# Kernel optimization log

Hardware: AMD Instinct MI355X
Metric: run time of the kernel (lower is better)

Reference implementation:

```python
import jax, jax.numpy as jnp
import numpy as np

H, C = 4, 64          # heads, per-head out_channels (hidden_dim // heads)
D = 256               # hidden_dim
DE = 128              # edge_dim
N_ROWS, N_TOKENS, E = 20000, 100000, 300000
SCALE = 1.0 / np.sqrt(C).astype(np.float32)
EPS = 1e-5


def _lin(key, din, dout):
    k1, k2 = jax.random.split(key)
    W = jax.random.normal(k1, (din, dout), jnp.float32) * 0.05
    b = jax.random.normal(k2, (dout,), jnp.float32) * 0.05
    return W, b


def setup_inputs() -> dict:
    key = jax.random.key(0)
    ks = jax.random.split(key, 26)
    inp = {
        "row_x": jax.random.normal(ks[0], (N_ROWS, D), jnp.float32),
        "token_x": jax.random.normal(ks[1], (N_TOKENS, D), jnp.float32),
        "t2r_edge_index": jax.random.randint(ks[2], (2, E), 0, N_ROWS, jnp.int64),
        "edge_attr_t2r": jax.random.normal(ks[3], (E, DE), jnp.float32),
        "r2t_edge_index": jax.random.randint(ks[4], (2, E), 0, N_ROWS, jnp.int64),
        "edge_attr_r2t": jax.random.normal(ks[5], (E, DE), jnp.float32),
    }
    i = 6
    for p in ("t2r", "r2t"):
        for nm, din in (("q", D), ("k", D), ("v", D), ("e", DE), ("s", D)):
            W, b = _lin(ks[i], din, D); i += 1
            inp[p + "_W" + nm] = W
            inp[p + "_b" + nm] = b
    inp["row_gamma"] = jnp.ones((D,), jnp.float32)
    inp["row_beta"] = jnp.zeros((D,), jnp.float32)
    inp["token_gamma"] = jnp.ones((D,), jnp.float32)
    inp["token_beta"] = jnp.zeros((D,), jnp.float32)
    return inp


def _transformer_conv(x_src, x_dst, ei, ea, Wq, bq, Wk, bk, Wv, bv, We, be, Ws, bs):
    """PyG TransformerConv (concat=True, root_weight=True, edge_dim set, eval)."""
    N = x_dst.shape[0]
    q = (x_dst @ Wq + bq).reshape(N, H, C)       # [N_dst,H,C]
    k = (x_src @ Wk + bk).reshape(-1, H, C)      # [N_src,H,C]
    v = (x_src @ Wv + bv).reshape(-1, H, C)
    e = (ea @ We + be).reshape(-1, H, C)         # [E,H,C]
    src, dst = ei[0], ei[1]
    kj = k[src] + e                              # key_j + edge
    logits = jnp.einsum('ehc,ehc->eh', q[dst], kj) * SCALE  # [E,H]
    amax = jax.ops.segment_max(logits, dst, num_segments=N)  # [N,H]
    ex = jnp.exp(logits - amax[dst])
    denom = jax.ops.segment_sum(ex, dst, num_segments=N)
    alpha = ex / denom[dst]                      # segment softmax over dst
    msg = jax.ops.segment_sum((v[src] + e) * alpha[..., None], dst, num_segments=N)
    return msg.reshape(N, H * C) + x_dst @ Ws + bs  # concat heads + skip lin


def _ln(x, g, b):
    m = jnp.mean(x, -1, keepdims=True)
    var = jnp.mean(jnp.square(x - m), -1, keepdims=True)
    return (x - m) * jax.lax.rsqrt(var + EPS) * g + b


def reference(row_x, token_x, t2r_edge_index, edge_attr_t2r, r2t_edge_index, edge_attr_r2t,
              t2r_Wq, t2r_bq, t2r_Wk, t2r_bk, t2r_Wv, t2r_bv, t2r_We, t2r_be, t2r_Ws, t2r_bs,
              r2t_Wq, r2t_bq, r2t_Wk, r2t_bk, r2t_Wv, r2t_bv, r2t_We, r2t_be, r2t_Ws, r2t_bs,
              row_gamma, row_beta, token_gamma, token_beta):
    row_msg = _transformer_conv(token_x, row_x, t2r_edge_index, edge_attr_t2r,
                                t2r_Wq, t2r_bq, t2r_Wk, t2r_bk, t2r_Wv, t2r_bv,
                                t2r_We, t2r_be, t2r_Ws, t2r_bs)
    row_out = _ln(row_x + row_msg, row_gamma, row_beta)
    tok_msg = _transformer_conv(row_out, token_x, r2t_edge_index, edge_attr_r2t,
                                r2t_Wq, r2t_bq, r2t_Wk, r2t_bk, r2t_Wv, r2t_bv,
                                r2t_We, r2t_be, r2t_Ws, r2t_bs)
    token_out = _ln(token_x + tok_msg, token_gamma, token_beta)
    return row_out, token_out
```

## Files before the change

### kernel.cpp

```cpp
#include <hip/hip_runtime.h>
#include <cstdint>
#include <cstddef>

#define NMAX 100000
#define EMAX 300000

typedef __bf16 bf16_t;
typedef __bf16 bf16x8 __attribute__((ext_vector_type(8)));
typedef float f32x4 __attribute__((ext_vector_type(4)));
typedef unsigned int u32;

__device__ unsigned short g_mega[(size_t)NMAX * 1024];
__device__ unsigned short g_qs [(size_t)NMAX * 512];
__device__ unsigned short g_kv [(size_t)NMAX * 512];
__device__ unsigned short g_eb1[(size_t)EMAX * 256];
__device__ unsigned short g_eb2[(size_t)EMAX * 256];
__device__ unsigned short g_bfA[(size_t)NMAX * 256];
__device__ unsigned short g_bfB[(size_t)NMAX * 256];
__device__ unsigned short g_bfW[589824];
__device__ float g_bias[2560];
__device__ int   g_deg [NMAX + 1];
__device__ int   g_rowptr[NMAX + 1];
__device__ int   g_cur [NMAX];
__device__ int2  g_perm2[EMAX];
__device__ int   g_bsum[512];

struct P4  { const float* p[4]; };
struct P10 { const float* p[10]; };

__device__ __forceinline__ unsigned short f2bf(float f) {
  unsigned u = __float_as_uint(f);
  return (unsigned short)((u + 0x7fffu + ((u >> 16) & 1u)) >> 16);
}
__device__ __forceinline__ void dec8(uint4 u, float* f) {
  f[0] = __uint_as_float(u.x << 16); f[1] = __uint_as_float(u.x & 0xffff0000u);
  f[2] = __uint_as_float(u.y << 16); f[3] = __uint_as_float(u.y & 0xffff0000u);
  f[4] = __uint_as_float(u.z << 16); f[5] = __uint_as_float(u.z & 0xffff0000u);
  f[6] = __uint_as_float(u.w << 16); f[7] = __uint_as_float(u.w & 0xffff0000u);
}

__global__ __launch_bounds__(256) void conv_bf16(const float* __restrict__ in,
                                                 unsigned short* __restrict__ out,
                                                 long long n8) {
  long long i = (long long)blockIdx.x * 256 + threadIdx.x;
  if (i >= n8) return;
  const float4* p = (const float4*)(in + i * 8);
  float4 a = p[0], b = p[1];
  ushort4 lo = make_ushort4(f2bf(a.x), f2bf(a.y), f2bf(a.z), f2bf(a.w));
  ushort4 hi = make_ushort4(f2bf(b.x), f2bf(b.y), f2bf(b.z), f2bf(b.w));
  ushort4* q = (ushort4*)(out + i * 8);
  q[0] = lo; q[1] = hi;
}

__global__ __launch_bounds__(256) void wconv4(P4 Ws, unsigned short* __restrict__ Wt,
                                              int K, int NN) {
  int i = blockIdx.x * 256 + threadIdx.x;
  if (i >= NN * K) return;
  int n = i / K, k = i - n * K;
  Wt[i] = f2bf(Ws.p[n >> 8][(size_t)k * 256 + (n & 255)]);
}

__global__ __launch_bounds__(256) void bconcat(P10 b, float* __restrict__ out) {
  int i = blockIdx.x * 256 + threadIdx.x;
  if (i < 2560) out[i] = b.p[i >> 8][i & 255];
}

#define GLL16(gp, lp) __builtin_amdgcn_global_load_lds( \
    (const __attribute__((address_space(1))) void*)(gp), \
    (__attribute__((address_space(3))) void*)(lp), 16, 0, 0)

template <int K, int NS, bool AF32>
__global__ __launch_bounds__(256) void gemm_mfma(const void* __restrict__ Av,
                                                 const unsigned short* __restrict__ Bt,
                                                 const float* __restrict__ bias,
                                                 unsigned short* __restrict__ C, int M) {
  constexpr int NC  = NS / 128;
  constexpr int LNC = (NC == 8) ? 3 : (NC == 4) ? 2 : 1;
  const int g = blockIdx.x;
  const int r8 = g & 7;
  const int cch = (g >> 3) & (NC - 1);
  const int q8 = g >> (3 + LNC);
  const int mt = q8 * 8 + r8;
  if (mt * 128 >= M) return;
  const int bm = mt * 128, bn = cch * 128;

  __shared__ __align__(16) unsigned short As[128 * 64];
  __shared__ __align__(16) unsigned short Bs[128 * 64];
  const int tid = threadIdx.x;
  const int lane = tid & 63, wid = tid >> 6;
  const int wrow = (wid & 1) * 64, wcol = (wid >> 1) * 64;
  const int sr = lane >> 3;
  const int slot = lane & 7;

  f32x4 acc[4][4] = {};

  for (int k0 = 0; k0 < K; k0 += 64) {
    {
#pragma unroll
      for (int r = 0; r < 4; ++r) {
        int col = (wid * 4 + r) * 8 + sr;
        int kk = k0 + ((slot ^ (col & 7)) << 3);
        GLL16(Bt + (size_t)(bn + col) * K + kk, (unsigned short*)Bs + (size_t)(wid * 4 + r) * 512);
      }
    }
    if constexpr (AF32) {
      const float* Af = (const float*)Av;
#pragma unroll
      for (int r = 0; r < 4; ++r) {
        int row = (wid * 4 + r) * 8 + sr;
        int arow = bm + row; if (arow >= M) arow = M - 1;
        int kk = k0 + ((slot ^ (row & 7)) << 3);
        const float* ap = Af + (size_t)arow * K + kk;
        float4 f0 = *(const float4*)ap;
        float4 f1 = *(const float4*)(ap + 4);
        bf16x8 a;
        a[0] = (bf16_t)f0.x; a[1] = (bf16_t)f0.y; a[2] = (bf16_t)f0.z; a[3] = (bf16_t)f0.w;
        a[4] = (bf16_t)f1.x; a[5] = (bf16_t)f1.y; a[6] = (bf16_t)f1.z; a[7] = (bf16_t)f1.w;
        *(bf16x8*)((char*)As + (size_t)row * 128 + (size_t)(slot << 4)) = a;
      }
    } else {
      const unsigned short* Af = (const unsigned short*)Av;
#pragma unroll
      for (int r = 0; r < 4; ++r) {
        int row = (wid * 4 + r) * 8 + sr;
        int arow = bm + row; if (arow >= M) arow = M - 1;
        int kk = k0 + ((slot ^ (row & 7)) << 3);
        GLL16(Af + (size_t)arow * K + kk, (unsigned short*)As + (size_t)(wid * 4 + r) * 512);
      }
    }
    __syncthreads();
    const char* Ab = (const char*)As;
    const char* Bb = (const char*)Bs;
#pragma unroll
    for (int h = 0; h < 2; ++h) {
      bf16x8 af[4], bfr[4];
      int g2 = (lane >> 4) + h * 4;
#pragma unroll
      for (int fm = 0; fm < 4; ++fm) {
        int row = wrow + fm * 16 + (lane & 15);
        af[fm] = *(const bf16x8*)(Ab + row * 128 + ((g2 ^ (row & 7)) << 4));
      }
#pragma unroll
      for (int fn = 0; fn < 4; ++fn) {
        int col = wcol + fn * 16 + (lane & 15);
        bfr[fn] = *(const bf16x8*)(Bb + col * 128 + ((g2 ^ (col & 7)) << 4));
      }
#pragma unroll
      for (int fm = 0; fm < 4; ++fm)
#pragma unroll
        for (int fn = 0; fn < 4; ++fn)
          acc[fm][fn] = __builtin_amdgcn_mfma_f32_16x16x32_bf16(af[fm], bfr[fn],
                                                                acc[fm][fn], 0, 0, 0);
    }
    __syncthreads();
  }
  float bv[4];
#pragma unroll
  for (int fn = 0; fn < 4; ++fn) bv[fn] = bias[bn + wcol + fn * 16 + (lane & 15)];
#pragma unroll
  for (int fm = 0; fm < 4; ++fm) {
    int rbase = bm + wrow + fm * 16 + ((lane >> 4) << 2);
#pragma unroll
    for (int j = 0; j < 4; ++j) {
      int row = rbase + j;
      if (row < M) {
        size_t rb = (size_t)row * NS + bn + wcol + (lane & 15);
#pragma unroll
        for (int fn = 0; fn < 4; ++fn)
          C[rb + fn * 16] = f2bf(acc[fm][fn][j] + bv[fn]);
      }
    }
  }
}

__global__ __launch_bounds__(256) void hist_kernel(const int* __restrict__ ei,
                                                   int* __restrict__ deg, int E) {
  int i = blockIdx.x * 256 + threadIdx.x;
  if (i < E) atomicAdd(&deg[ei[E + i]], 1);
}

__global__ __launch_bounds__(256) void scan1(const int* __restrict__ deg,
                                             int* __restrict__ rowptr,
                                             int* __restrict__ bsum, int n) {
  __shared__ int ws[4];
  int i = blockIdx.x * 256 + threadIdx.x;
  int v = (i < n) ? deg[i] : 0;
  int lane = threadIdx.x & 63, wid = threadIdx.x >> 6;
  int inc = v;
#pragma unroll
  for (int o = 1; o < 64; o <<= 1) {
    int t = __shfl_up(inc, o);
    if (lane >= o) inc += t;
  }
  if (lane == 63) ws[wid] = inc;
  __syncthreads();
  int woff = 0;
  if (wid > 0) woff += ws[0];
  if (wid > 1) woff += ws[1];
  if (wid > 2) woff += ws[2];
  if (i < n) rowptr[i] = inc - v + woff;
  if (threadIdx.x == 255) bsum[blockIdx.x] = inc + woff;
}

__global__ __launch_bounds__(512) void scan2(int* __restrict__ bsum, int B) {
  __shared__ int s[512];
  int t = threadIdx.x;
  int v = (t < B) ? bsum[t] : 0;
  s[t] = v;
  __syncthreads();
  for (int o = 1; o < 512; o <<= 1) {
    int a = (t >= o) ? s[t - o] : 0;
    __syncthreads();
    s[t] += a;
    __syncthreads();
  }
  if (t < B) bsum[t] = s[t] - v;
}

__global__ __launch_bounds__(256) void scan3(int* __restrict__ rowptr,
                                             const int* __restrict__ bsum,
                                             const int* __restrict__ deg,
                                             int* __restrict__ cur, int n) {
  int i = blockIdx.x * 256 + threadIdx.x;
  if (i < n) {
    int r = rowptr[i] + bsum[blockIdx.x];
    rowptr[i] = r;
    cur[i] = r;
    if (i == n - 1) rowptr[n] = r + deg[i];
  }
}

__global__ __launch_bounds__(256) void scatter_kernel(const int* __restrict__ ei,
                                                      int* __restrict__ cur,
                                                      int2* __restrict__ perm2, int E) {
  int i = blockIdx.x * 256 + threadIdx.x;
  if (i < E) {
    int s = ei[i];
    int d = ei[E + i];
    int pos = atomicAdd(&cur[d], 1);
    perm2[pos] = make_int2(s, i);
  }
}

__global__ __launch_bounds__(256) void fused_attn_ln(
    const int* __restrict__ rowptr, const int2* __restrict__ perm2,
    const unsigned short* __restrict__ qs, int qs_stride,
    const unsigned short* __restrict__ kv, int kv_stride,
    const unsigned short* __restrict__ eb,
    const float* __restrict__ x,
    const float* __restrict__ gamma, const float* __restrict__ beta,
    float* __restrict__ out, unsigned short* __restrict__ out_bf, int N) {
  int node = blockIdx.x * 8 + (threadIdx.x >> 5);
  if (node >= N) return;
  int sub = threadIdx.x & 31;
  int c8 = sub << 3;
  uint4 qu = *(const uint4*)(qs + (size_t)node * qs_stride + c8);
  uint4 su = *(const uint4*)(qs + (size_t)node * qs_stride + 256 + c8);
  size_t base = (size_t)node * 256 + c8;
  float4 xv0 = *(const float4*)(x + base);
  float4 xv1 = *(const float4*)(x + base + 4);
  float q[8], s[8];
  dec8(qu, q); dec8(su, s);
  float acc[8] = {0.f, 0.f, 0.f, 0.f, 0.f, 0.f, 0.f, 0.f};
  float m = -1e30f, den = 0.f;
  int beg = rowptr[node], end = rowptr[node + 1];
  int2 se = (beg < end) ? perm2[beg] : make_int2(0, 0);
  uint4 ku = *(const uint4*)(kv + (size_t)se.x * kv_stride + c8);
  uint4 vu = *(const uint4*)(kv + (size_t)se.x * kv_stride + 256 + c8);
  uint4 eu = *(const uint4*)(eb + (size_t)se.y * 256 + c8);
  for (int p_ = beg; p_ < end; ++p_) {
    int2 seN = (p_ + 1 < end) ? perm2[p_ + 1] : se;
    uint4 kuN = *(const uint4*)(kv + (size_t)seN.x * kv_stride + c8);
    uint4 vuN = *(const uint4*)(kv + (size_t)seN.x * kv_stride + 256 + c8);
    uint4 euN = *(const uint4*)(eb + (size_t)seN.y * 256 + c8);
    float kf[8], vf[8], ef[8];
    dec8(ku, kf); dec8(vu, vf); dec8(eu, ef);
    float p = 0.f;
#pragma unroll
    for (int j = 0; j < 8; ++j) p += q[j] * (kf[j] + ef[j]);
    p += __shfl_xor(p, 1); p += __shfl_xor(p, 2); p += __shfl_xor(p, 4);
    p *= 0.125f;
    float mn = fmaxf(m, p);
    float sc = expf(m - mn);
    float w  = expf(p - mn);
    den = den * sc + w;
#pragma unroll
    for (int j = 0; j < 8; ++j) acc[j] = acc[j] * sc + w * (vf[j] + ef[j]);
    m = mn;
    ku = kuN; vu = vuN; eu = euN; se = seN;
  }
  float inv = (den > 0.f) ? 1.0f / den : 0.f;
  float val[8];
  val[0] = xv0.x + s[0] + acc[0] * inv; val[1] = xv0.y + s[1] + acc[1] * inv;
  val[2] = xv0.z + s[2] + acc[2] * inv; val[3] = xv0.w + s[3] + acc[3] * inv;
  val[4] = xv1.x + s[4] + acc[4] * inv; val[5] = xv1.y + s[5] + acc[5] * inv;
  val[6] = xv1.z + s[6] + acc[6] * inv; val[7] = xv1.w + s[7] + acc[7] * inv;
  float t = 0.f;
#pragma unroll
  for (int j = 0; j < 8; ++j) t += val[j];
#pragma unroll
  for (int o = 1; o < 32; o <<= 1) t += __shfl_xor(t, o);
  float mean = t * (1.0f / 256.0f);
  float d[8], ss = 0.f;
#pragma unroll
  for (int j = 0; j < 8; ++j) { d[j] = val[j] - mean; ss += d[j] * d[j]; }
#pragma unroll
  for (int o = 1; o < 32; o <<= 1) ss += __shfl_xor(ss, o);
  float rstd = rsqrtf(ss * (1.0f / 256.0f) + 1e-5f);
  float4 g0 = *(const float4*)(gamma + c8);
  float4 g1 = *(const float4*)(gamma + c8 + 4);
  float4 b0 = *(const float4*)(beta + c8);
  float4 b1 = *(const float4*)(beta + c8 + 4);
  float o8[8];
  o8[0] = d[0] * rstd * g0.x + b0.x; o8[1] = d[1] * rstd * g0.y + b0.y;
  o8[2] = d[2] * rstd * g0.z + b0.z; o8[3] = d[3] * rstd * g0.w + b0.w;
  o8[4] = d[4] * rstd * g1.x + b1.x; o8[5] = d[5] * rstd * g1.y + b1.y;
  o8[6] = d[6] * rstd * g1.z + b1.z; o8[7] = d[7] * rstd * g1.w + b1.w;
  *(float4*)(out + base)     = make_float4(o8[0], o8[1], o8[2], o8[3]);
  *(float4*)(out + base + 4) = make_float4(o8[4], o8[5], o8[6], o8[7]);
  if (out_bf) {
    uint4 ob;
    ob.x = (u32)f2bf(o8[0]) | ((u32)f2bf(o8[1]) << 16);
    ob.y = (u32)f2bf(o8[2]) | ((u32)f2bf(o8[3]) << 16);
    ob.z = (u32)f2bf(o8[4]) | ((u32)f2bf(o8[5]) << 16);
    ob.w = (u32)f2bf(o8[6]) | ((u32)f2bf(o8[7]) << 16);
    *(uint4*)(out_bf + base) = ob;
  }
}

extern "C" void kernel_launch(void* const* d_in, const int* in_sizes, int n_in,
                              void* d_out, int out_size, void* d_ws, size_t ws_size,
                              hipStream_t stream) {
  const float* row_x   = (const float*)d_in[0];
  const float* token_x = (const float*)d_in[1];
  const int*   ei1     = (const int*)d_in[2];
  const float* ea1     = (const float*)d_in[3];
  const int*   ei2     = (const int*)d_in[4];
  const float* ea2     = (const float*)d_in[5];

  const float* W1q = (const float*)d_in[6];  const float* b1q = (const float*)d_in[7];
  const float* W1k = (const float*)d_in[8];  const float* b1k = (const float*)d_in[9];
  const float* W1v = (const float*)d_in[10]; const float* b1v = (const float*)d_in[11];
  const float* W1e = (const float*)d_in[12]; const float* b1e = (const float*)d_in[13];
  const float* W1s = (const float*)d_in[14]; const float* b1s = (const float*)d_in[15];
  const float* W2q = (const float*)d_in[16]; const float* b2q = (const float*)d_in[17];
  const float* W2k = (const float*)d_in[18]; const float* b2k = (const float*)d_in[19];
  const float* W2v = (const float*)d_in[20]; const float* b2v = (const float*)d_in[21];
  const float* W2e = (const float*)d_in[22]; const float* b2e = (const float*)d_in[23];
  const float* W2s = (const float*)d_in[24]; const float* b2s = (const float*)d_in[25];
  const float* row_gamma   = (const float*)d_in[26];
  const float* row_beta    = (const float*)d_in[27];
  const float* token_gamma = (const float*)d_in[28];
  const float* token_beta  = (const float*)d_in[29];

  const int NR = in_sizes[0] / 256;
  const int NT = in_sizes[1] / 256;
  const int E  = in_sizes[2] / 2;

  float* out_row = (float*)d_out;
  float* out_tok = (float*)d_out + (long long)NR * 256;

  void *pmega_, *pqs_, *pkv_, *peb1_, *peb2_, *pbfA_, *pbfB_,
       *pbfW_, *pbias_, *pdeg_, *prp_, *pcur_, *pperm_, *pbs_;
  hipGetSymbolAddress(&pmega_, HIP_SYMBOL(g_mega));
  hipGetSymbolAddress(&pqs_,   HIP_SYMBOL(g_qs));
  hipGetSymbolAddress(&pkv_,   HIP_SYMBOL(g_kv));
  hipGetSymbolAddress(&peb1_,  HIP_SYMBOL(g_eb1));
  hipGetSymbolAddress(&peb2_,  HIP_SYMBOL(g_eb2));
  hipGetSymbolAddress(&pbfA_,  HIP_SYMBOL(g_bfA));
  hipGetSymbolAddress(&pbfB_,  HIP_SYMBOL(g_bfB));
  hipGetSymbolAddress(&pbfW_,  HIP_SYMBOL(g_bfW));
  hipGetSymbolAddress(&pbias_, HIP_SYMBOL(g_bias));
  hipGetSymbolAddress(&pdeg_,  HIP_SYMBOL(g_deg));
  hipGetSymbolAddress(&prp_,   HIP_SYMBOL(g_rowptr));
  hipGetSymbolAddress(&pcur_,  HIP_SYMBOL(g_cur));
  hipGetSymbolAddress(&pperm_, HIP_SYMBOL(g_perm2));
  hipGetSymbolAddress(&pbs_,   HIP_SYMBOL(g_bsum));
  unsigned short* mega = (unsigned short*)pmega_;
  unsigned short* qs   = (unsigned short*)pqs_;
  unsigned short* kv   = (unsigned short*)pkv_;
  unsigned short* eb1  = (unsigned short*)peb1_;
  unsigned short* eb2  = (unsigned short*)peb2_;
  unsigned short* bfA  = (unsigned short*)pbfA_;
  unsigned short* bfB  = (unsigned short*)pbfB_;
  unsigned short* bfW  = (unsigned short*)pbfW_;
  float* gbias = (float*)pbias_;
  int*   deg   = (int*)pdeg_;
  int*   rp    = (int*)prp_;
  int*   cur   = (int*)pcur_;
  int2*  perm2 = (int2*)pperm_;
  int*   bsum  = (int*)pbs_;

  unsigned short* Wmega = bfW + 0;
  unsigned short* Wqs1  = bfW + 262144;
  unsigned short* Wkv2  = bfW + 393216;
  unsigned short* We1   = bfW + 524288;
  unsigned short* We2   = bfW + 557056;
  wconv4<<<1024, 256, 0, stream>>>(P4{{W1k, W1v, W2q, W2s}}, Wmega, 256, 1024);
  wconv4<<<512, 256, 0, stream>>>(P4{{W1q, W1s, nullptr, nullptr}}, Wqs1, 256, 512);
  wconv4<<<512, 256, 0, stream>>>(P4{{W2k, W2v, nullptr, nullptr}}, Wkv2, 256, 512);
  wconv4<<<128, 256, 0, stream>>>(P4{{W1e, nullptr, nullptr, nullptr}}, We1, 128, 256);
  wconv4<<<128, 256, 0, stream>>>(P4{{W2e, nullptr, nullptr, nullptr}}, We2, 128, 256);
  P10 bp{{b1k, b1v, b2q, b2s, b1q, b1s, b2k, b2v, b1e, b2e}};
  bconcat<<<10, 256, 0, stream>>>(bp, gbias);

  conv_bf16<<<(int)(((long long)NT * 32 + 255) / 256), 256, 0, stream>>>(
      token_x, bfA, (long long)NT * 32);

  const int egrid = (E + 255) / 256;

  auto csr = [&](const int* ei, int Ndst) {
    hipMemsetAsync(deg, 0, (size_t)(Ndst + 1) * sizeof(int), stream);
    hist_kernel<<<egrid, 256, 0, stream>>>(ei, deg, E);
    int B = (Ndst + 255) / 256;
    scan1<<<B, 256, 0, stream>>>(deg, rp, bsum, Ndst);
    scan2<<<1, 512, 0, stream>>>(bsum, B);
    scan3<<<B, 256, 0, stream>>>(rp, bsum, deg, cur, Ndst);
    scatter_kernel<<<egrid, 256, 0, stream>>>(ei, cur, perm2, E);
  };

  auto swgrid = [](int M, int NC) {
    int nm = (M + 127) / 128;
    return (((nm + 7) / 8) * 8) * NC;
  };

  gemm_mfma<256, 1024, false><<<swgrid(NT, 8), 256, 0, stream>>>(
      bfA, Wmega, gbias + 0, mega, NT);
  gemm_mfma<256, 512, true><<<swgrid(NR, 4), 256, 0, stream>>>(
      row_x, Wqs1, gbias + 1024, qs, NR);
  gemm_mfma<128, 256, true><<<swgrid(E, 2), 256, 0, stream>>>(
      ea1, We1, gbias + 2048, eb1, E);
  gemm_mfma<128, 256, true><<<swgrid(E, 2), 256, 0, stream>>>(
      ea2, We2, gbias + 2304, eb2, E);

  csr(ei1, NR);
  fused_attn_ln<<<(NR + 7) / 8, 256, 0, stream>>>(rp, perm2,
                                                  qs, 512, mega, 1024, eb1,
                                                  row_x, row_gamma, row_beta,
                                                  out_row, bfB, NR);

  gemm_mfma<256, 512, false><<<swgrid(NR, 4), 256, 0, stream>>>(
      bfB, Wkv2, gbias + 1536, kv, NR);
  csr(ei2, NT);
  fused_attn_ln<<<(NT + 7) / 8, 256, 0, stream>>>(rp, perm2,
                                                  mega + 512, 1024, kv, 512, eb2,
                                                  token_x, token_gamma, token_beta,
                                                  out_tok, nullptr, NT);
}
```

Baseline: 653.1 us.

## Skip mega-GEMM row tiles beyond maximum referenced edge index

Adds a kernel that computes the maximum source index of the first edge set and the maximum destination index of the second using wave reductions and atomics. The fused token GEMM then skips row tiles beyond those bounds for the K/V and Q2 column chunks, since those rows are never gathered. The skip projection columns are still computed for every row. This removes unused GEMM work at the cost of an extra small kernel and memset.

```diff
diff --git a/kernel.cpp b/kernel.cpp
--- a/kernel.cpp
+++ b/kernel.cpp
@@ -24,6 +24,7 @@
 __device__ int   g_cur [NMAX];
 __device__ int2  g_perm2[EMAX];
 __device__ int   g_bsum[512];
+__device__ int   g_bounds[2];
 
 struct P4  { const float* p[4]; };
 struct P10 { const float* p[10]; };
@@ -65,15 +66,33 @@
   if (i < 2560) out[i] = b.p[i >> 8][i & 255];
 }
 
+__global__ __launch_bounds__(256) void edge_bounds(const int* __restrict__ s1,
+                                                   const int* __restrict__ d2,
+                                                   int E, int* __restrict__ b) {
+  int i = blockIdx.x * 256 + threadIdx.x;
+  int v0 = (i < E) ? s1[i] : 0;
+  int v1 = (i < E) ? d2[i] : 0;
+#pragma unroll
+  for (int o = 32; o; o >>= 1) {
+    v0 = max(v0, __shfl_xor(v0, o));
+    v1 = max(v1, __shfl_xor(v1, o));
+  }
+  if ((threadIdx.x & 63) == 0) {
+    atomicMax(&b[0], v0);
+    atomicMax(&b[1], v1);
+  }
+}
+
 #define GLL16(gp, lp) __builtin_amdgcn_global_load_lds( \
     (const __attribute__((address_space(1))) void*)(gp), \
     (__attribute__((address_space(3))) void*)(lp), 16, 0, 0)
 
-template <int K, int NS, bool AF32>
+template <int K, int NS, bool AF32, bool GATED>
 __global__ __launch_bounds__(256) void gemm_mfma(const void* __restrict__ Av,
                                                  const unsigned short* __restrict__ Bt,
                                                  const float* __restrict__ bias,
-                                                 unsigned short* __restrict__ C, int M) {
+                                                 unsigned short* __restrict__ C, int M,
+                                                 const int* __restrict__ bnd) {
   constexpr int NC  = NS / 128;
   constexpr int LNC = (NC == 8) ? 3 : (NC == 4) ? 2 : 1;
   const int g = blockIdx.x;
@@ -83,6 +102,10 @@
   const int mt = q8 * 8 + r8;
   if (mt * 128 >= M) return;
   const int bm = mt * 128, bn = cch * 128;
+  if constexpr (GATED) {
+    int lim = (cch < 4) ? bnd[0] : ((cch < 6) ? bnd[1] : 0x7fffffff);
+    if (bm > lim) return;
+  }
 
   __shared__ __align__(16) unsigned short As[128 * 64];
   __shared__ __align__(16) unsigned short Bs[128 * 64];
@@ -361,7 +384,7 @@
   float* out_tok = (float*)d_out + (long long)NR * 256;
 
   void *pmega_, *pqs_, *pkv_, *peb1_, *peb2_, *pbfA_, *pbfB_,
-       *pbfW_, *pbias_, *pdeg_, *prp_, *pcur_, *pperm_, *pbs_;
+       *pbfW_, *pbias_, *pdeg_, *prp_, *pcur_, *pperm_, *pbs_, *pbnd_;
   hipGetSymbolAddress(&pmega_, HIP_SYMBOL(g_mega));
   hipGetSymbolAddress(&pqs_,   HIP_SYMBOL(g_qs));
   hipGetSymbolAddress(&pkv_,   HIP_SYMBOL(g_kv));
@@ -376,6 +399,7 @@
   hipGetSymbolAddress(&pcur_,  HIP_SYMBOL(g_cur));
   hipGetSymbolAddress(&pperm_, HIP_SYMBOL(g_perm2));
   hipGetSymbolAddress(&pbs_,   HIP_SYMBOL(g_bsum));
+  hipGetSymbolAddress(&pbnd_,  HIP_SYMBOL(g_bounds));
   unsigned short* mega = (unsigned short*)pmega_;
   unsigned short* qs   = (unsigned short*)pqs_;
   unsigned short* kv   = (unsigned short*)pkv_;
@@ -390,6 +414,7 @@
   int*   cur   = (int*)pcur_;
   int2*  perm2 = (int2*)pperm_;
   int*   bsum  = (int*)pbs_;
+  int*   bnd   = (int*)pbnd_;
 
   unsigned short* Wmega = bfW + 0;
   unsigned short* Wqs1  = bfW + 262144;
@@ -404,10 +429,13 @@
   P10 bp{{b1k, b1v, b2q, b2s, b1q, b1s, b2k, b2v, b1e, b2e}};
   bconcat<<<10, 256, 0, stream>>>(bp, gbias);
 
+  const int egrid = (E + 255) / 256;
+
+  hipMemsetAsync(bnd, 0, 2 * sizeof(int), stream);
+  edge_bounds<<<egrid, 256, 0, stream>>>(ei1, ei2 + E, E, bnd);
+
   conv_bf16<<<(int)(((long long)NT * 32 + 255) / 256), 256, 0, stream>>>(
       token_x, bfA, (long long)NT * 32);
-
-  const int egrid = (E + 255) / 256;
 
   auto csr = [&](const int* ei, int Ndst) {
     hipMemsetAsync(deg, 0, (size_t)(Ndst + 1) * sizeof(int), stream);
@@ -424,14 +452,14 @@
     return (((nm + 7) / 8) * 8) * NC;
   };
 
-  gemm_mfma<256, 1024, false><<<swgrid(NT, 8), 256, 0, stream>>>(
-      bfA, Wmega, gbias + 0, mega, NT);
-  gemm_mfma<256, 512, true><<<swgrid(NR, 4), 256, 0, stream>>>(
-      row_x, Wqs1, gbias + 1024, qs, NR);
-  gemm_mfma<128, 256, true><<<swgrid(E, 2), 256, 0, stream>>>(
-      ea1, We1, gbias + 2048, eb1, E);
-  gemm_mfma<128, 256, true><<<swgrid(E, 2), 256, 0, stream>>>(
-      ea2, We2, gbias + 2304, eb2, E);
+  gemm_mfma<256, 1024, false, true><<<swgrid(NT, 8), 256, 0, stream>>>(
+      bfA, Wmega, gbias + 0, mega, NT, bnd);
+  gemm_mfma<256, 512, true, false><<<swgrid(NR, 4), 256, 0, stream>>>(
+      row_x, Wqs1, gbias + 1024, qs, NR, nullptr);
+  gemm_mfma<128, 256, true, false><<<swgrid(E, 2), 256, 0, stream>>>(
+      ea1, We1, gbias + 2048, eb1, E, nullptr);
+  gemm_mfma<128, 256, true, false><<<swgrid(E, 2), 256, 0, stream>>>(
+      ea2, We2, gbias + 2304, eb2, E, nullptr);
 
   csr(ei1, NR);
   fused_attn_ln<<<(NR + 7) / 8, 256, 0, stream>>>(rp, perm2,
@@ -439,8 +467,8 @@
                                                   row_x, row_gamma, row_beta,
                                                   out_row, bfB, NR);
 
-  gemm_mfma<256, 512, false><<<swgrid(NR, 4), 256, 0, stream>>>(
-      bfB, Wkv2, gbias + 1536, kv, NR);
+  gemm_mfma<256, 512, false, false><<<swgrid(NR, 4), 256, 0, stream>>>(
+      bfB, Wkv2, gbias + 1536, kv, NR, nullptr);
   csr(ei2, NT);
   fused_attn_ln<<<(NT + 7) / 8, 256, 0, stream>>>(rp, perm2,
                                                   mega + 512, 1024, kv, 512, eb2,
```

New measurement: 717.2 us. 9.8% more time.

## Write edge projections in CSR order so attention reads them sequentially

Applied to the files above, without the earlier changes.

Both CSR builds now run before the GEMMs, and the scatter kernel records each edge's sorted position. The edge-attribute GEMM epilogue uses that inverse permutation to write each projected edge row at its CSR slot. The attention kernel then reads edge features contiguously by position instead of gathering them by original edge id, and the perm array shrinks from int2 to int. The cost is scattered row writes in the GEMM epilogue, an extra index load per output row, and separate CSR buffers for the two convolutions.

```diff
diff --git a/kernel.cpp b/kernel.cpp
--- a/kernel.cpp
+++ b/kernel.cpp
@@ -20,9 +20,13 @@
 __device__ unsigned short g_bfW[589824];
 __device__ float g_bias[2560];
 __device__ int   g_deg [NMAX + 1];
-__device__ int   g_rowptr[NMAX + 1];
+__device__ int   g_rp1 [NMAX + 1];
+__device__ int   g_rp2 [NMAX + 1];
 __device__ int   g_cur [NMAX];
-__device__ int2  g_perm2[EMAX];
+__device__ int   g_ps1 [EMAX];
+__device__ int   g_ps2 [EMAX];
+__device__ int   g_inv1[EMAX];
+__device__ int   g_inv2[EMAX];
 __device__ int   g_bsum[512];
 
 struct P4  { const float* p[4]; };
@@ -73,7 +77,8 @@
 __global__ __launch_bounds__(256) void gemm_mfma(const void* __restrict__ Av,
                                                  const unsigned short* __restrict__ Bt,
                                                  const float* __restrict__ bias,
-                                                 unsigned short* __restrict__ C, int M) {
+                                                 unsigned short* __restrict__ C, int M,
+                                                 const int* __restrict__ inv) {
   constexpr int NC  = NS / 128;
   constexpr int LNC = (NC == 8) ? 3 : (NC == 4) ? 2 : 1;
   const int g = blockIdx.x;
@@ -164,7 +169,8 @@
     for (int j = 0; j < 4; ++j) {
       int row = rbase + j;
       if (row < M) {
-        size_t rb = (size_t)row * NS + bn + wcol + (lane & 15);
+        size_t orow = inv ? (size_t)inv[row] : (size_t)row;
+        size_t rb = orow * NS + bn + wcol + (lane & 15);
 #pragma unroll
         for (int fn = 0; fn < 4; ++fn)
           C[rb + fn * 16] = f2bf(acc[fm][fn][j] + bv[fn]);
@@ -232,18 +238,20 @@
 
 __global__ __launch_bounds__(256) void scatter_kernel(const int* __restrict__ ei,
                                                       int* __restrict__ cur,
-                                                      int2* __restrict__ perm2, int E) {
+                                                      int* __restrict__ psrc,
+                                                      int* __restrict__ inv, int E) {
   int i = blockIdx.x * 256 + threadIdx.x;
   if (i < E) {
     int s = ei[i];
     int d = ei[E + i];
     int pos = atomicAdd(&cur[d], 1);
-    perm2[pos] = make_int2(s, i);
+    psrc[pos] = s;
+    inv[i] = pos;
   }
 }
 
 __global__ __launch_bounds__(256) void fused_attn_ln(
-    const int* __restrict__ rowptr, const int2* __restrict__ perm2,
+    const int* __restrict__ rowptr, const int* __restrict__ psrc,
     const unsigned short* __restrict__ qs, int qs_stride,
     const unsigned short* __restrict__ kv, int kv_stride,
     const unsigned short* __restrict__ eb,
@@ -264,15 +272,16 @@
   float acc[8] = {0.f, 0.f, 0.f, 0.f, 0.f, 0.f, 0.f, 0.f};
   float m = -1e30f, den = 0.f;
   int beg = rowptr[node], end = rowptr[node + 1];
-  int2 se = (beg < end) ? perm2[beg] : make_int2(0, 0);
-  uint4 ku = *(const uint4*)(kv + (size_t)se.x * kv_stride + c8);
-  uint4 vu = *(const uint4*)(kv + (size_t)se.x * kv_stride + 256 + c8);
-  uint4 eu = *(const uint4*)(eb + (size_t)se.y * 256 + c8);
+  int src = (beg < end) ? psrc[beg] : 0;
+  uint4 ku = *(const uint4*)(kv + (size_t)src * kv_stride + c8);
+  uint4 vu = *(const uint4*)(kv + (size_t)src * kv_stride + 256 + c8);
+  uint4 eu = *(const uint4*)(eb + (size_t)((beg < end) ? beg : 0) * 256 + c8);
   for (int p_ = beg; p_ < end; ++p_) {
-    int2 seN = (p_ + 1 < end) ? perm2[p_ + 1] : se;
-    uint4 kuN = *(const uint4*)(kv + (size_t)seN.x * kv_stride + c8);
-    uint4 vuN = *(const uint4*)(kv + (size_t)seN.x * kv_stride + 256 + c8);
-    uint4 euN = *(const uint4*)(eb + (size_t)seN.y * 256 + c8);
+    int pn = (p_ + 1 < end) ? (p_ + 1) : p_;
+    int srcN = psrc[pn];
+    uint4 kuN = *(const uint4*)(kv + (size_t)srcN * kv_stride + c8);
+    uint4 vuN = *(const uint4*)(kv + (size_t)srcN * kv_stride + 256 + c8);
+    uint4 euN = *(const uint4*)(eb + (size_t)pn * 256 + c8);
     float kf[8], vf[8], ef[8];
     dec8(ku, kf); dec8(vu, vf); dec8(eu, ef);
     float p = 0.f;
@@ -287,7 +296,7 @@
 #pragma unroll
     for (int j = 0; j < 8; ++j) acc[j] = acc[j] * sc + w * (vf[j] + ef[j]);
     m = mn;
-    ku = kuN; vu = vuN; eu = euN; se = seN;
+    ku = kuN; vu = vuN; eu = euN;
   }
   float inv = (den > 0.f) ? 1.0f / den : 0.f;
   float val[8];
@@ -360,8 +369,8 @@
   float* out_row = (float*)d_out;
   float* out_tok = (float*)d_out + (long long)NR * 256;
 
-  void *pmega_, *pqs_, *pkv_, *peb1_, *peb2_, *pbfA_, *pbfB_,
-       *pbfW_, *pbias_, *pdeg_, *prp_, *pcur_, *pperm_, *pbs_;
+  void *pmega_, *pqs_, *pkv_, *peb1_, *peb2_, *pbfA_, *pbfB_, *pbfW_, *pbias_,
+       *pdeg_, *prp1_, *prp2_, *pcur_, *pps1_, *pps2_, *pinv1_, *pinv2_, *pbs_;
   hipGetSymbolAddress(&pmega_, HIP_SYMBOL(g_mega));
   hipGetSymbolAddress(&pqs_,   HIP_SYMBOL(g_qs));
   hipGetSymbolAddress(&pkv_,   HIP_SYMBOL(g_kv));
@@ -372,9 +381,13 @@
   hipGetSymbolAddress(&pbfW_,  HIP_SYMBOL(g_bfW));
   hipGetSymbolAddress(&pbias_, HIP_SYMBOL(g_bias));
   hipGetSymbolAddress(&pdeg_,  HIP_SYMBOL(g_deg));
-  hipGetSymbolAddress(&prp_,   HIP_SYMBOL(g_rowptr));
+  hipGetSymbolAddress(&prp1_,  HIP_SYMBOL(g_rp1));
+  hipGetSymbolAddress(&prp2_,  HIP_SYMBOL(g_rp2));
   hipGetSymbolAddress(&pcur_,  HIP_SYMBOL(g_cur));
-  hipGetSymbolAddress(&pperm_, HIP_SYMBOL(g_perm2));
+  hipGetSymbolAddress(&pps1_,  HIP_SYMBOL(g_ps1));
+  hipGetSymbolAddress(&pps2_,  HIP_SYMBOL(g_ps2));
+  hipGetSymbolAddress(&pinv1_, HIP_SYMBOL(g_inv1));
+  hipGetSymbolAddress(&pinv2_, HIP_SYMBOL(g_inv2));
   hipGetSymbolAddress(&pbs_,   HIP_SYMBOL(g_bsum));
   unsigned short* mega = (unsigned short*)pmega_;
   unsigned short* qs   = (unsigned short*)pqs_;
@@ -386,9 +399,13 @@
   unsigned short* bfW  = (unsigned short*)pbfW_;
   float* gbias = (float*)pbias_;
   int*   deg   = (int*)pdeg_;
-  int*   rp    = (int*)prp_;
+  int*   rp1   = (int*)prp1_;
+  int*   rp2   = (int*)prp2_;
   int*   cur   = (int*)pcur_;
-  int2*  perm2 = (int2*)pperm_;
+  int*   ps1   = (int*)pps1_;
+  int*   ps2   = (int*)pps2_;
+  int*   inv1  = (int*)pinv1_;
+  int*   inv2  = (int*)pinv2_;
   int*   bsum  = (int*)pbs_;
 
   unsigned short* Wmega = bfW + 0;
@@ -409,15 +426,18 @@
 
   const int egrid = (E + 255) / 256;
 
-  auto csr = [&](const int* ei, int Ndst) {
+  auto csr = [&](const int* ei, int Ndst, int* rp, int* psrc, int* inv) {
     hipMemsetAsync(deg, 0, (size_t)(Ndst + 1) * sizeof(int), stream);
     hist_kernel<<<egrid, 256, 0, stream>>>(ei, deg, E);
     int B = (Ndst + 255) / 256;
     scan1<<<B, 256, 0, stream>>>(deg, rp, bsum, Ndst);
     scan2<<<1, 512, 0, stream>>>(bsum, B);
     scan3<<<B, 256, 0, stream>>>(rp, bsum, deg, cur, Ndst);
-    scatter_kernel<<<egrid, 256, 0, stream>>>(ei, cur, perm2, E);
+    scatter_kernel<<<egrid, 256, 0, stream>>>(ei, cur, psrc, inv, E);
   };
+
+  csr(ei1, NR, rp1, ps1, inv1);
+  csr(ei2, NT, rp2, ps2, inv2);
 
   auto swgrid = [](int M, int NC) {
     int nm = (M + 127) / 128;
@@ -425,24 +445,22 @@
   };
 
   gemm_mfma<256, 1024, false><<<swgrid(NT, 8), 256, 0, stream>>>(
-      bfA, Wmega, gbias + 0, mega, NT);
+      bfA, Wmega, gbias + 0, mega, NT, nullptr);
   gemm_mfma<256, 512, true><<<swgrid(NR, 4), 256, 0, stream>>>(
-      row_x, Wqs1, gbias + 1024, qs, NR);
+      row_x, Wqs1, gbias + 1024, qs, NR, nullptr);
   gemm_mfma<128, 256, true><<<swgrid(E, 2), 256, 0, stream>>>(
-      ea1, We1, gbias + 2048, eb1, E);
+      ea1, We1, gbias + 2048, eb1, E, inv1);
   gemm_mfma<128, 256, true><<<swgrid(E, 2), 256, 0, stream>>>(
-      ea2, We2, gbias + 2304, eb2, E);
-
-  csr(ei1, NR);
-  fused_attn_ln<<<(NR + 7) / 8, 256, 0, stream>>>(rp, perm2,
+      ea2, We2, gbias + 2304, eb2, E, inv2);
+
+  fused_attn_ln<<<(NR + 7) / 8, 256, 0, stream>>>(rp1, ps1,
                                                   qs, 512, mega, 1024, eb1,
                                                   row_x, row_gamma, row_beta,
                                                   out_row, bfB, NR);
 
   gemm_mfma<256, 512, false><<<swgrid(NR, 4), 256, 0, stream>>>(
-      bfB, Wkv2, gbias + 1536, kv, NR);
-  csr(ei2, NT);
-  fused_attn_ln<<<(NT + 7) / 8, 256, 0, stream>>>(rp, perm2,
+      bfB, Wkv2, gbias + 1536, kv, NR, nullptr);
+  fused_attn_ln<<<(NT + 7) / 8, 256, 0, stream>>>(rp2, ps2,
                                                   mega + 512, 1024, kv, 512, eb2,
                                                   token_x, token_gamma, token_beta,
                                                   out_tok, nullptr, NT);
```

Result: faster. 634.8 us (-2.8%).
